# Kernel tuning notes

Measured on AMD Instinct MI355X. Metric: run time of the kernel, lower is better.

The kernel has to match this reference:

```python
import jax, jax.numpy as jnp
import numpy as np

B, C, H, W = 32, 512, 32, 32
INNER = C // 8


def setup_inputs() -> dict:
    key = jax.random.key(0)
    k_x, k_f, k_g, k_h = jax.random.split(key, 4)
    x = jax.random.normal(k_x, (B, C, H, W), dtype=jnp.float32)
    # 1x1 Conv1d weights (bias=False) are plain [out, in] matrices.
    s_in = 1.0 / np.sqrt(C)
    Wf = jax.random.uniform(k_f, (INNER, C), dtype=jnp.float32, minval=-s_in, maxval=s_in)
    Wg = jax.random.uniform(k_g, (INNER, C), dtype=jnp.float32, minval=-s_in, maxval=s_in)
    Wh = jax.random.uniform(k_h, (C, C), dtype=jnp.float32, minval=-s_in, maxval=s_in)
    return {"x": x, "Wf": Wf, "Wg": Wg, "Wh": Wh}


def reference(x, Wf, Wg, Wh):
    b, c = x.shape[0], x.shape[1]
    xf = x.reshape(b, c, -1)                       # [B, C, N]
    f = jnp.einsum('ic,bcn->bin', Wf, xf)          # [B, inner, N]
    g = jnp.einsum('ic,bcn->bin', Wg, xf)          # [B, inner, N]
    h = jnp.einsum('oc,bcn->bon', Wh, xf)          # [B, C, N]
    sim = jnp.einsum('bin,bim->bnm', f, g)         # f^T g -> [B, N, N]
    beta = jax.nn.softmax(sim, axis=1)             # softmax over the f-index axis (dim=1)
    o = jnp.einsum('bcn,bnm->bcm', h, beta)        # [B, C, N]
    return o
```

## Files before the change

### kernel.cpp

```cpp
#include <hip/hip_runtime.h>
#include <stdint.h>

#define CDIM 512
#define NPIX 1024
#define IDIM 64

#define WS_BATCH (65536 + 65536 + 524288)
#define XT_OFF   ((size_t)32 * WS_BATCH)
#define XT_ELEMS ((size_t)32 * 1024 * 512)
#define WH_OFF   (XT_OFF + XT_ELEMS)
#define P_OFF    XT_OFF
#define P_ELEMS  ((size_t)32 * 1024 * 1024)
#define LP_OFF   (P_OFF + P_ELEMS)

typedef __bf16 bf16x8 __attribute__((ext_vector_type(8)));
typedef _Float16 f16x8 __attribute__((ext_vector_type(8)));
typedef float f32x4 __attribute__((ext_vector_type(4)));
typedef unsigned short u16x8 __attribute__((ext_vector_type(8)));

__device__ __forceinline__ unsigned short f2bf(float f) {
    union { float f; uint32_t u; } v; v.f = f;
    uint32_t u = v.u;
    u += 0x7fffu + ((u >> 16) & 1u);
    return (unsigned short)(u >> 16);
}

__device__ __forceinline__ f32x4 mfma_bf(bf16x8 a, bf16x8 b, f32x4 c) {
    return __builtin_amdgcn_mfma_f32_16x16x32_bf16(a, b, c, 0, 0, 0);
}
__device__ __forceinline__ f32x4 mfma_h(f16x8 a, f16x8 b, f32x4 c) {
    return __builtin_amdgcn_mfma_f32_16x16x32_f16(a, b, c, 0, 0, 0);
}
__device__ __forceinline__ void gld_lds16(const void* g, void* l) {
    __builtin_amdgcn_global_load_lds(
        (const __attribute__((address_space(1))) unsigned int*)g,
        (__attribute__((address_space(3))) unsigned int*)l,
        16, 0, 0);
}
__device__ __forceinline__ void barrier_mem() {
    asm volatile("" ::: "memory");
    __builtin_amdgcn_s_barrier();
    asm volatile("" ::: "memory");
}
__device__ __forceinline__ int swz(int by) { return by ^ (((by >> 7) & 3) << 4); }

__global__ __launch_bounds__(256) void xw_cvt(
    const float* __restrict__ x,
    const float* __restrict__ Wf, const float* __restrict__ Wg,
    const float* __restrict__ Wh,
    _Float16* __restrict__ xT, _Float16* __restrict__ wh)
{
    const int t = threadIdx.x;
    if (blockIdx.y == 8) {
        int wb = blockIdx.z * 16 + blockIdx.x;
        if (wb >= 320) return;
        int e = (wb * 256 + t) * 4;
        int r = e >> 9, k = e & 511;
        const float* src;
        if (r < 64)       src = Wf + (size_t)r * 512 + k;
        else if (r < 128) src = Wg + (size_t)(r - 64) * 512 + k;
        else              src = Wh + (size_t)(r - 128) * 512 + k;
        float4 v = *(const float4*)src;
        _Float16 h4[4] = {(_Float16)v.x, (_Float16)v.y, (_Float16)v.z, (_Float16)v.w};
        *(ushort4*)(wh + e) = *(ushort4*)h4;
        return;
    }
    __shared__ _Float16 tile[64][72];
    const int b = blockIdx.z, c0 = blockIdx.y * 64, n0 = blockIdx.x * 64;
    const float* xb = x + ((size_t)b * CDIM + c0) * NPIX + n0;
    #pragma unroll
    for (int p = 0; p < 4; ++p) {
        int ci = p * 16 + (t >> 4);
        int nj = (t & 15) * 4;
        float4 v = *(const float4*)(xb + (size_t)ci * NPIX + nj);
        tile[nj + 0][ci] = (_Float16)v.x;
        tile[nj + 1][ci] = (_Float16)v.y;
        tile[nj + 2][ci] = (_Float16)v.z;
        tile[nj + 3][ci] = (_Float16)v.w;
    }
    __syncthreads();
    _Float16* dst = xT + ((size_t)b * NPIX + n0) * CDIM + c0;
    #pragma unroll
    for (int p = 0; p < 2; ++p) {
        int n  = p * 32 + (t >> 3);
        int cc = (t & 7) * 8;
        ushort4 a  = *(ushort4*)&tile[n][cc];
        ushort4 bq = *(ushort4*)&tile[n][cc + 4];
        *(ushort4*)(dst + (size_t)n * CDIM + cc)     = a;
        *(ushort4*)(dst + (size_t)n * CDIM + cc + 4) = bq;
    }
}

__global__ __launch_bounds__(256, 4) void fgh_mfma(
    const _Float16* __restrict__ wh, const _Float16* __restrict__ xT,
    unsigned short* __restrict__ ws)
{
    const int orig = blockIdx.x;
    const int work = (orig & 7) * 160 + (orig >> 3);
    const int b    = work / 40;
    const int tile = work % 40;
    const int tr = tile >> 3, tn = tile & 7;

    const int t = threadIdx.x, lane = t & 63, w = t >> 6;
    const int lr = lane & 15, lg = lane >> 4;
    const int wr = w >> 1, wc = w & 1;

    __shared__ __align__(16) char smem[36864];

    const _Float16* Ag = wh + (size_t)(tr * 128) * CDIM;
    const _Float16* Bg = xT + ((size_t)b * NPIX + tn * 128) * CDIM;

    int offA[4], offB[4];
    #pragma unroll
    for (int mf = 0; mf < 4; ++mf)
        offA[mf] = swz((wr * 64 + mf * 16 + lr) * 64 + lg * 16);
    #pragma unroll
    for (int nf = 0; nf < 4; ++nf)
        offB[nf] = swz((wc * 64 + nf * 16 + lr) * 64 + lg * 16);

    f32x4 acc[4][4];
    #pragma unroll
    for (int i = 0; i < 4; ++i)
        #pragma unroll
        for (int j = 0; j < 4; ++j) acc[i][j] = (f32x4){0.f, 0.f, 0.f, 0.f};

    auto stage = [&](int buf, int k0) {
        #pragma unroll
        for (int p = 0; p < 2; ++p) {
            int q = p * 256 + t;
            gld_lds16(Ag + (size_t)(q >> 2) * CDIM + k0 + ((q & 3) ^ ((q >> 3) & 3)) * 8,
                      smem + buf * 8192 + q * 16);
        }
        #pragma unroll
        for (int p = 0; p < 2; ++p) {
            int q = p * 256 + t;
            gld_lds16(Bg + (size_t)(q >> 2) * CDIM + k0 + ((q & 3) ^ ((q >> 3) & 3)) * 8,
                      smem + 16384 + buf * 8192 + q * 16);
        }
    };

    stage(0, 0);
    stage(1, 32);

    #pragma unroll 1
    for (int ks = 0; ks < 16; ++ks) {
        const int cur = ks & 1;
        if (ks < 15) asm volatile("s_waitcnt vmcnt(4)" ::: "memory");
        else         asm volatile("s_waitcnt vmcnt(0)" ::: "memory");
        barrier_mem();

        const char* Ab = smem + cur * 8192;
        const char* Bb = smem + 16384 + cur * 8192;
        f16x8 af[4];
        #pragma unroll
        for (int mf = 0; mf < 4; ++mf)
            af[mf] = *(const f16x8*)(Ab + offA[mf]);
        #pragma unroll
        for (int nf = 0; nf < 4; ++nf) {
            f16x8 bv = *(const f16x8*)(Bb + offB[nf]);
            #pragma unroll
            for (int mf = 0; mf < 4; ++mf)
                acc[mf][nf] = mfma_h(af[mf], bv, acc[mf][nf]);
        }

        barrier_mem();
        if (ks + 2 < 16) stage(cur, (ks + 2) * 32);
    }

    unsigned short* base = ws + (size_t)b * WS_BATCH;
    const int nbase = tn * 128 + wc * 64;
    if (tr == 0) {
        unsigned short* dst = base + (wr ? 65536 : 0);
        #pragma unroll
        for (int mf = 0; mf < 4; ++mf) {
            const int i0 = mf * 16 + lg * 4;
            #pragma unroll
            for (int nf = 0; nf < 4; ++nf) {
                int n = nbase + nf * 16 + lr;
                ushort4 v;
                v.x = f2bf(acc[mf][nf][0]); v.y = f2bf(acc[mf][nf][1]);
                v.z = f2bf(acc[mf][nf][2]); v.w = f2bf(acc[mf][nf][3]);
                *(ushort4*)(dst + (size_t)n * 64 + i0) = v;
            }
        }
    } else {
        unsigned short* sc = (unsigned short*)smem + w * 4608;
        #pragma unroll
        for (int mf = 0; mf < 4; ++mf)
            #pragma unroll
            for (int nf = 0; nf < 4; ++nf)
                #pragma unroll
                for (int j = 0; j < 4; ++j)
                    sc[(mf * 16 + lg * 4 + j) * 72 + nf * 16 + lr] =
                        f2bf(acc[mf][nf][j]);
        unsigned short* hd = base + 131072;
        const int cbase = (tr - 1) * 128 + wr * 64;
        #pragma unroll
        for (int ii = 0; ii < 8; ++ii) {
            int cl = ii * 8 + (lane >> 3);
            int nl = (lane & 7) * 8;
            u16x8 v = *(const u16x8*)&sc[cl * 72 + nl];
            *(u16x8*)(hd + (size_t)(cbase + cl) * NPIX + nbase + nl) = v;
        }
    }
}

__global__ __launch_bounds__(256, 3) void attn_sm(
    const unsigned short* __restrict__ ws, unsigned short* __restrict__ P,
    float* __restrict__ Lp)
{
    const int orig = blockIdx.x;
    const int work = (orig & 7) * 256 + (orig >> 3);
    const int b    = work >> 6;
    const int tile = work & 63;
    const int mt = tile >> 2, nt = tile & 3;
    const int m0 = mt * 64, n0 = nt * 256;

    const int t = threadIdx.x, lane = t & 63, w = t >> 6;
    const int lr = lane & 15, lg = lane >> 4;

    const unsigned short* fT = ws + (size_t)b * WS_BATCH;
    const unsigned short* gT = fT + 65536;

    __shared__ unsigned short Ab[2][64 * 32];
    __shared__ unsigned short Bb[2][256 * 32];
    __shared__ float red[4][64];
    __shared__ unsigned short rp[4][16][72];

    #pragma unroll
    for (int kc = 0; kc < 2; ++kc) {
        {
            int q = t;
            gld_lds16(gT + (size_t)(m0 + (q >> 2)) * 64 + kc * 32 + ((q & 3) ^ ((q >> 3) & 3)) * 8,
                      (char*)&Ab[kc][0] + q * 16);
        }
        #pragma unroll
        for (int p = 0; p < 4; ++p) {
            int q = p * 256 + t;
            gld_lds16(fT + (size_t)(n0 + (q >> 2)) * 64 + kc * 32 + ((q & 3) ^ ((q >> 3) & 3)) * 8,
                      (char*)&Bb[kc][0] + q * 16);
        }
    }
    __syncthreads();

    int offA[4], offB[4];
    #pragma unroll
    for (int mf = 0; mf < 4; ++mf)
        offA[mf] = swz((mf * 16 + lr) * 64 + lg * 16);
    #pragma unroll
    for (int nf = 0; nf < 4; ++nf)
        offB[nf] = swz((w * 64 + nf * 16 + lr) * 64 + lg * 16);

    f32x4 acc[4][4];
    #pragma unroll
    for (int i = 0; i < 4; ++i)
        #pragma unroll
        for (int j = 0; j < 4; ++j) acc[i][j] = (f32x4){0.f, 0.f, 0.f, 0.f};

    #pragma unroll
    for (int kc = 0; kc < 2; ++kc) {
        const char* Abc = (const char*)&Ab[kc][0];
        const char* Bbc = (const char*)&Bb[kc][0];
        bf16x8 af[4];
        #pragma unroll
        for (int mf = 0; mf < 4; ++mf)
            af[mf] = *(const bf16x8*)(Abc + offA[mf]);
        #pragma unroll
        for (int nf = 0; nf < 4; ++nf) {
            bf16x8 bv = *(const bf16x8*)(Bbc + offB[nf]);
            #pragma unroll
            for (int mf = 0; mf < 4; ++mf)
                acc[mf][nf] = mfma_bf(af[mf], bv, acc[mf][nf]);
        }
    }

    #pragma unroll
    for (int mf = 0; mf < 4; ++mf) {
        #pragma unroll
        for (int j = 0; j < 4; ++j) {
            float s = 0.f;
            #pragma unroll
            for (int nf = 0; nf < 4; ++nf) {
                float e = __expf(acc[mf][nf][j]);
                acc[mf][nf][j] = e;
                s += e;
            }
            s += __shfl_xor(s, 1);
            s += __shfl_xor(s, 2);
            s += __shfl_xor(s, 4);
            s += __shfl_xor(s, 8);
            if (lr == 0) red[w][mf * 16 + lg * 4 + j] = s;
        }
    }
    __syncthreads();
    if (t < 64) {
        float s = red[0][t] + red[1][t] + red[2][t] + red[3][t];
        Lp[(size_t)nt * 32768 + (size_t)b * 1024 + m0 + t] = s;
    }

    unsigned short* Pb = P + (size_t)b * NPIX * NPIX;
    #pragma unroll
    for (int mf = 0; mf < 4; ++mf) {
        #pragma unroll
        for (int nf = 0; nf < 4; ++nf)
            #pragma unroll
            for (int j = 0; j < 4; ++j)
                rp[w][lg * 4 + j][nf * 16 + lr] = f2bf(acc[mf][nf][j]);
        #pragma unroll
        for (int ii = 0; ii < 2; ++ii) {
            int row = ii * 8 + (lane >> 3);
            int ch  = lane & 7;
            ushort4 v0 = *(ushort4*)&rp[w][row][ch * 8];
            ushort4 v1 = *(ushort4*)&rp[w][row][ch * 8 + 4];
            unsigned short* dst = Pb + (size_t)(m0 + mf * 16 + row) * NPIX
                                     + n0 + w * 64 + ch * 8;
            *(ushort4*)(dst)     = v0;
            *(ushort4*)(dst + 4) = v1;
        }
    }
}

__global__ __launch_bounds__(512, 2) void attn_pv(
    const unsigned short* __restrict__ P, const unsigned short* __restrict__ ws,
    const float* __restrict__ Lp, float* __restrict__ out)
{
    const int orig = blockIdx.x;
    const int work = (orig & 7) * 32 + (orig >> 3);
    const int b    = work >> 3;
    const int tile = work & 7;
    const int m0   = (tile >> 1) * 256;
    const int c0   = (tile & 1) * 256;

    const int t = threadIdx.x, lane = t & 63, w = t >> 6;
    const int lr = lane & 15, lg = lane >> 4;
    const int wr = w >> 2, wc = w & 3;

    __shared__ __align__(16) char smem[131072];

    const unsigned short* Ag = P + ((size_t)b * NPIX + m0) * NPIX;
    const unsigned short* Bg = ws + (size_t)b * WS_BATCH + 131072 + (size_t)c0 * NPIX;

    const int sk0 = ((lg) ^ (lr & 7)) * 16;
    const int sk1 = ((4 + lg) ^ (lr & 7)) * 16;
    const int rAbase = (wr * 128 + lr) * 128;
    const int rBbase = (wc * 64 + lr) * 128;

    f32x4 acc[8][4];
    #pragma unroll
    for (int i = 0; i < 8; ++i)
        #pragma unroll
        for (int j = 0; j < 4; ++j) acc[i][j] = (f32x4){0.f, 0.f, 0.f, 0.f};

    auto stage_half = [&](int buf, int isB, int half, int kt) {
        const unsigned short* G = isB ? Bg : Ag;
        char* L = smem + isB * 65536 + buf * 32768 + half * 16384;
        #pragma unroll
        for (int l = 0; l < 2; ++l) {
            int q = l * 512 + t;
            gld_lds16(G + (size_t)(half * 128 + (q >> 3)) * NPIX + kt * 64
                        + (((q & 7) ^ ((q >> 3) & 7)) * 8),
                      L + q * 16);
        }
    };

    stage_half(0, 0, 0, 0); stage_half(0, 0, 1, 0);
    stage_half(0, 1, 0, 0); stage_half(0, 1, 1, 0);
    stage_half(1, 1, 0, 1); stage_half(1, 1, 1, 1);
    asm volatile("s_waitcnt vmcnt(4)" ::: "memory");
    barrier_mem();

    bf16x8 bfr[4][2];

    #pragma unroll 1
    for (int j = 0; j < 8; ++j) {
        const bool nl = (j < 7);
        #pragma unroll
        for (int grp = 0; grp < 2; ++grp) {
            const char* Abase = smem + grp * 32768;
            const char* Bbase = smem + 65536 + grp * 32768;
            #pragma unroll
            for (int p = 0; p < 4; ++p) {
                if (p == 0) {
                    #pragma unroll
                    for (int nf = 0; nf < 4; ++nf) {
                        bfr[nf][0] = *(const bf16x8*)(Bbase + rBbase + nf * 2048 + sk0);
                        bfr[nf][1] = *(const bf16x8*)(Bbase + rBbase + nf * 2048 + sk1);
                    }
                }
                bf16x8 af[2][2];
                #pragma unroll
                for (int e = 0; e < 2; ++e) {
                    af[e][0] = *(const bf16x8*)(Abase + rAbase + (p * 2 + e) * 2048 + sk0);
                    af[e][1] = *(const bf16x8*)(Abase + rAbase + (p * 2 + e) * 2048 + sk1);
                }
                if (grp == 0) {
                    if (p == 0) stage_half(1, 0, 0, 2 * j + 1);
                    if (p == 1) stage_half(1, 0, 1, 2 * j + 1);
                    if (p == 2 && nl) stage_half(0, 1, 0, 2 * j + 2);
                    if (p == 3 && nl) stage_half(0, 1, 1, 2 * j + 2);
                } else {
                    if (p == 0 && nl) stage_half(0, 0, 0, 2 * j + 2);
                    if (p == 1 && nl) stage_half(0, 0, 1, 2 * j + 2);
                    if (p == 2 && nl) stage_half(1, 1, 0, 2 * j + 3);
                    if (p == 3 && nl) stage_half(1, 1, 1, 2 * j + 3);
                }
                if (p == 3) {
                    if (nl) asm volatile("s_waitcnt vmcnt(4)" ::: "memory");
                    else    asm volatile("s_waitcnt vmcnt(0)" ::: "memory");
                }
                barrier_mem();
                __builtin_amdgcn_s_setprio(1);
                #pragma unroll
                for (int ks = 0; ks < 2; ++ks)
                    #pragma unroll
                    for (int e = 0; e < 2; ++e)
                        #pragma unroll
                        for (int nf = 0; nf < 4; ++nf)
                            acc[p * 2 + e][nf] =
                                mfma_bf(af[e][ks], bfr[nf][ks], acc[p * 2 + e][nf]);
                __builtin_amdgcn_s_setprio(0);
            }
        }
    }

    #pragma unroll
    for (int mf = 0; mf < 8; ++mf) {
        const size_t mi = (size_t)b * 1024 + m0 + wr * 128 + mf * 16 + lg * 4;
        f32x4 L = *(const f32x4*)&Lp[mi]
                + *(const f32x4*)&Lp[32768 + mi]
                + *(const f32x4*)&Lp[65536 + mi]
                + *(const f32x4*)&Lp[98304 + mi];
        f32x4 rinv;
        #pragma unroll
        for (int j = 0; j < 4; ++j) rinv[j] = 1.0f / L[j];
        #pragma unroll
        for (int nf = 0; nf < 4; ++nf) {
            f32x4 o = acc[mf][nf] * rinv;
            int c = c0 + wc * 64 + nf * 16 + lr;
            int m = m0 + wr * 128 + mf * 16 + lg * 4;
            *(f32x4*)(out + ((size_t)b * CDIM + c) * NPIX + m) = o;
        }
    }
}

extern "C" void kernel_launch(void* const* d_in, const int* in_sizes, int n_in,
                              void* d_out, int out_size, void* d_ws, size_t ws_size,
                              hipStream_t stream) {
    const float* x  = (const float*)d_in[0];
    const float* Wf = (const float*)d_in[1];
    const float* Wg = (const float*)d_in[2];
    const float* Wh = (const float*)d_in[3];
    unsigned short* ws = (unsigned short*)d_ws;
    _Float16* xT = (_Float16*)(ws + XT_OFF);
    _Float16* wh = (_Float16*)(ws + WH_OFF);
    unsigned short* P = ws + P_OFF;
    float* Lp = (float*)(ws + LP_OFF);
    float* out = (float*)d_out;

    xw_cvt<<<dim3(16, 9, 32), 256, 0, stream>>>(x, Wf, Wg, Wh, xT, wh);
    fgh_mfma<<<1280, 256, 0, stream>>>(wh, xT, ws);
    attn_sm<<<2048, 256, 0, stream>>>(ws, P, Lp);
    attn_pv<<<256, 512, 0, stream>>>(P, ws, Lp, out);
}
```

Before: 113.2 us.

## Shrink PV output tile to 128x256 and switch to triple-buffered LDS pipeline

The attn_pv kernel moves from 256 blocks with 256x256 output tiles to 512 blocks with 128x256 tiles. Each K-step now stages A and B together into a three-deep LDS ring, so loads run two steps ahead. The aim is to fill all CUs with twice the blocks and to simplify the prefetch schedule. The trade-off is less reuse per block, so P is read the same number of times but the V operand is read twice as often, and LDS per block grows to 144KB.

```diff
diff --git a/kernel.cpp b/kernel.cpp
--- a/kernel.cpp
+++ b/kernel.cpp
@@ -325,107 +325,110 @@
     const float* __restrict__ Lp, float* __restrict__ out)
 {
     const int orig = blockIdx.x;
-    const int work = (orig & 7) * 32 + (orig >> 3);
-    const int b    = work >> 3;
-    const int tile = work & 7;
-    const int m0   = (tile >> 1) * 256;
-    const int c0   = (tile & 1) * 256;
+    const int rnd  = orig >> 8;
+    const int o2   = orig & 255;
+    const int wk   = (o2 & 7) * 32 + (o2 >> 3);
+    const int b    = wk >> 3;
+    const int m0   = (wk & 7) * 128;
+    const int c0   = rnd * 256;
 
     const int t = threadIdx.x, lane = t & 63, w = t >> 6;
     const int lr = lane & 15, lg = lane >> 4;
     const int wr = w >> 2, wc = w & 3;
 
-    __shared__ __align__(16) char smem[131072];
+    __shared__ __align__(16) char smem[147456];
 
     const unsigned short* Ag = P + ((size_t)b * NPIX + m0) * NPIX;
     const unsigned short* Bg = ws + (size_t)b * WS_BATCH + 131072 + (size_t)c0 * NPIX;
 
     const int sk0 = ((lg) ^ (lr & 7)) * 16;
     const int sk1 = ((4 + lg) ^ (lr & 7)) * 16;
-    const int rAbase = (wr * 128 + lr) * 128;
+    const int rAbase = (wr * 64 + lr) * 128;
     const int rBbase = (wc * 64 + lr) * 128;
 
-    f32x4 acc[8][4];
-    #pragma unroll
-    for (int i = 0; i < 8; ++i)
+    f32x4 acc[4][4];
+    #pragma unroll
+    for (int i = 0; i < 4; ++i)
         #pragma unroll
         for (int j = 0; j < 4; ++j) acc[i][j] = (f32x4){0.f, 0.f, 0.f, 0.f};
 
-    auto stage_half = [&](int buf, int isB, int half, int kt) {
-        const unsigned short* G = isB ? Bg : Ag;
-        char* L = smem + isB * 65536 + buf * 32768 + half * 16384;
+    auto stage = [&](int kt) {
+        const int buf = kt % 3;
+        char* La = smem + buf * 16384;
+        char* Lb = smem + 49152 + buf * 32768;
         #pragma unroll
         for (int l = 0; l < 2; ++l) {
             int q = l * 512 + t;
-            gld_lds16(G + (size_t)(half * 128 + (q >> 3)) * NPIX + kt * 64
+            gld_lds16(Ag + (size_t)(q >> 3) * NPIX + kt * 64
                         + (((q & 7) ^ ((q >> 3) & 7)) * 8),
-                      L + q * 16);
+                      La + q * 16);
+        }
+        #pragma unroll
+        for (int l = 0; l < 4; ++l) {
+            int q = l * 512 + t;
+            gld_lds16(Bg + (size_t)(q >> 3) * NPIX + kt * 64
+                        + (((q & 7) ^ ((q >> 3) & 7)) * 8),
+                      Lb + q * 16);
         }
     };
 
-    stage_half(0, 0, 0, 0); stage_half(0, 0, 1, 0);
-    stage_half(0, 1, 0, 0); stage_half(0, 1, 1, 0);
-    stage_half(1, 1, 0, 1); stage_half(1, 1, 1, 1);
-    asm volatile("s_waitcnt vmcnt(4)" ::: "memory");
+    stage(0);
+    stage(1);
+    asm volatile("s_waitcnt vmcnt(6)" ::: "memory");
     barrier_mem();
 
-    bf16x8 bfr[4][2];
-
     #pragma unroll 1
-    for (int j = 0; j < 8; ++j) {
-        const bool nl = (j < 7);
-        #pragma unroll
-        for (int grp = 0; grp < 2; ++grp) {
-            const char* Abase = smem + grp * 32768;
-            const char* Bbase = smem + 65536 + grp * 32768;
-            #pragma unroll
-            for (int p = 0; p < 4; ++p) {
-                if (p == 0) {
-                    #pragma unroll
-                    for (int nf = 0; nf < 4; ++nf) {
-                        bfr[nf][0] = *(const bf16x8*)(Bbase + rBbase + nf * 2048 + sk0);
-                        bfr[nf][1] = *(const bf16x8*)(Bbase + rBbase + nf * 2048 + sk1);
-                    }
-                }
-                bf16x8 af[2][2];
+    for (int kt = 0; kt < 16; ++kt) {
+        const char* Ab = smem + (kt % 3) * 16384;
+        const char* Bb = smem + 49152 + (kt % 3) * 32768;
+
+        bf16x8 bfr[4][2];
+        #pragma unroll
+        for (int nf = 0; nf < 4; ++nf) {
+            bfr[nf][0] = *(const bf16x8*)(Bb + rBbase + nf * 2048 + sk0);
+            bfr[nf][1] = *(const bf16x8*)(Bb + rBbase + nf * 2048 + sk1);
+        }
+        bf16x8 af0[2][2];
+        #pragma unroll
+        for (int e = 0; e < 2; ++e) {
+            af0[e][0] = *(const bf16x8*)(Ab + rAbase + e * 2048 + sk0);
+            af0[e][1] = *(const bf16x8*)(Ab + rAbase + e * 2048 + sk1);
+        }
+        if (kt + 2 < 16) stage(kt + 2);
+        barrier_mem();
+        __builtin_amdgcn_s_setprio(1);
+        #pragma unroll
+        for (int ks = 0; ks < 2; ++ks)
+            #pragma unroll
+            for (int e = 0; e < 2; ++e)
                 #pragma unroll
-                for (int e = 0; e < 2; ++e) {
-                    af[e][0] = *(const bf16x8*)(Abase + rAbase + (p * 2 + e) * 2048 + sk0);
-                    af[e][1] = *(const bf16x8*)(Abase + rAbase + (p * 2 + e) * 2048 + sk1);
-                }
-                if (grp == 0) {
-                    if (p == 0) stage_half(1, 0, 0, 2 * j + 1);
-                    if (p == 1) stage_half(1, 0, 1, 2 * j + 1);
-                    if (p == 2 && nl) stage_half(0, 1, 0, 2 * j + 2);
-                    if (p == 3 && nl) stage_half(0, 1, 1, 2 * j + 2);
-                } else {
-                    if (p == 0 && nl) stage_half(0, 0, 0, 2 * j + 2);
-                    if (p == 1 && nl) stage_half(0, 0, 1, 2 * j + 2);
-                    if (p == 2 && nl) stage_half(1, 1, 0, 2 * j + 3);
-                    if (p == 3 && nl) stage_half(1, 1, 1, 2 * j + 3);
-                }
-                if (p == 3) {
-                    if (nl) asm volatile("s_waitcnt vmcnt(4)" ::: "memory");
-                    else    asm volatile("s_waitcnt vmcnt(0)" ::: "memory");
-                }
-                barrier_mem();
-                __builtin_amdgcn_s_setprio(1);
+                for (int nf = 0; nf < 4; ++nf)
+                    acc[e][nf] = mfma_bf(af0[e][ks], bfr[nf][ks], acc[e][nf]);
+        __builtin_amdgcn_s_setprio(0);
+
+        bf16x8 af1[2][2];
+        #pragma unroll
+        for (int e = 0; e < 2; ++e) {
+            af1[e][0] = *(const bf16x8*)(Ab + rAbase + (2 + e) * 2048 + sk0);
+            af1[e][1] = *(const bf16x8*)(Ab + rAbase + (2 + e) * 2048 + sk1);
+        }
+        if (kt <= 13) asm volatile("s_waitcnt vmcnt(6)" ::: "memory");
+        else          asm volatile("s_waitcnt vmcnt(0)" ::: "memory");
+        barrier_mem();
+        __builtin_amdgcn_s_setprio(1);
+        #pragma unroll
+        for (int ks = 0; ks < 2; ++ks)
+            #pragma unroll
+            for (int e = 0; e < 2; ++e)
                 #pragma unroll
-                for (int ks = 0; ks < 2; ++ks)
-                    #pragma unroll
-                    for (int e = 0; e < 2; ++e)
-                        #pragma unroll
-                        for (int nf = 0; nf < 4; ++nf)
-                            acc[p * 2 + e][nf] =
-                                mfma_bf(af[e][ks], bfr[nf][ks], acc[p * 2 + e][nf]);
-                __builtin_amdgcn_s_setprio(0);
-            }
-        }
-    }
-
-    #pragma unroll
-    for (int mf = 0; mf < 8; ++mf) {
-        const size_t mi = (size_t)b * 1024 + m0 + wr * 128 + mf * 16 + lg * 4;
+                for (int nf = 0; nf < 4; ++nf)
+                    acc[2 + e][nf] = mfma_bf(af1[e][ks], bfr[nf][ks], acc[2 + e][nf]);
+        __builtin_amdgcn_s_setprio(0);
+    }
+
+    #pragma unroll
+    for (int mf = 0; mf < 4; ++mf) {
+        const size_t mi = (size_t)b * 1024 + m0 + wr * 64 + mf * 16 + lg * 4;
         f32x4 L = *(const f32x4*)&Lp[mi]
                 + *(const f32x4*)&Lp[32768 + mi]
                 + *(const f32x4*)&Lp[65536 + mi]
@@ -437,7 +440,7 @@
         for (int nf = 0; nf < 4; ++nf) {
             f32x4 o = acc[mf][nf] * rinv;
             int c = c0 + wc * 64 + nf * 16 + lr;
-            int m = m0 + wr * 128 + mf * 16 + lg * 4;
+            int m = m0 + wr * 64 + mf * 16 + lg * 4;
             *(f32x4*)(out + ((size_t)b * CDIM + c) * NPIX + m) = o;
         }
     }
@@ -460,5 +463,5 @@
     xw_cvt<<<dim3(16, 9, 32), 256, 0, stream>>>(x, Wf, Wg, Wh, xT, wh);
     fgh_mfma<<<1280, 256, 0, stream>>>(wh, xT, ws);
     attn_sm<<<2048, 256, 0, stream>>>(ws, P, Lp);
-    attn_pv<<<256, 512, 0, stream>>>(P, ws, Lp, out);
-}
+    attn_pv<<<512, 512, 0, stream>>>(P, ws, Lp, out);
+}
```

Measured after the change: 121.2 us. 1.07x slower.
